# Performance work log

Measured on AMD Instinct MI355X. Metric: run time of the kernel, lower is better.

## Reference

```python
import jax, jax.numpy as jnp
import numpy as np

# Module hyperparameters (from init_kwargs)
B, C, E, T = 8, 128, 128, 128          # batch, in_channels, embedding(freq), time
O, G, KW, KS = 256, 4, 9, 1            # out_channels, groups, kernel_width, kernel_stride
D = C // G                              # kernel depth per group = 32
N = O // G                              # filters per group = 64
AH, AS = 2, 2                           # activate_height, activate_stride
NEG_SLOPE = 0.01                        # nn.LeakyReLU default


def setup_inputs() -> dict:
    key = jax.random.key(0)
    kx, kw = jax.random.split(key)
    x = jax.random.normal(kx, (B, C, E, T), dtype=jnp.float32)
    # xavier_uniform over (O, D, E, KW): fan_in = D*E*KW, fan_out = O*E*KW
    fan_in, fan_out = D * E * KW, O * E * KW
    limit = float(np.sqrt(6.0 / (fan_in + fan_out)))
    weight = jax.random.uniform(kw, (O, D, E, KW), dtype=jnp.float32,
                                minval=-limit, maxval=limit)
    return {"x": x, "weight": weight}


def reference(x, weight):
    b, c, e, t = x.shape
    # --- symmetric-ish zero pad along time so unfold yields exactly t windows ---
    pad = (t - 1) * KS - t + KW
    xp = jnp.pad(x, ((0, 0), (0, 0), (0, 0), (pad // 2, (pad + 1) // 2)))
    # --- unfold: windows of size KW at stride KS -> (b, c, e, t, KW) ---
    idx = jnp.arange(t)[:, None] * KS + jnp.arange(KW)[None, :]  # (t, KW)
    xu = xp[..., idx]                                            # (b, c, e, t, KW)
    # --- grouped linear-conv: instead of materializing (b,t,g,n,d,e,KW), contract d,KW ---
    xu = xu.reshape(b, G, D, e, t, KW)                 # (b, g, d, e, t, w)
    wr = weight.reshape(G, N, D, e, KW)                # (g, n, d, e, w)
    # z[b,g,n,e,t] = sum_{d,w} xu * wr  (the all-ones conv sums over d and full width w)
    z = jnp.einsum('bgdetw,gndew->bgnet', xu, wr).reshape(b, O, e, t)
    # --- all-ones conv height pooling: kernel AH, stride AS over e (valid) ---
    f_out = (e - AH) // AS + 1
    cs = jnp.cumsum(z, axis=2)
    cs = jnp.concatenate([jnp.zeros_like(cs[:, :, :1]), cs], axis=2)  # prefix sums
    pos = jnp.arange(f_out) * AS
    pooled = cs[:, :, pos + AH, :] - cs[:, :, pos, :]   # (b, O, f_out, t)
    # --- LeakyReLU ---
    y = jnp.where(pooled >= 0, pooled, NEG_SLOPE * pooled)
    return y  # (b, o, f_out, t), matching 'b o f t'
```

## Files before the change

kernel.cpp:

```cpp
#include <hip/hip_runtime.h>
#include <cstddef>

typedef __attribute__((ext_vector_type(8))) short short8v;
typedef __attribute__((ext_vector_type(4))) float f32x4;

__device__ __forceinline__ unsigned short f2bf(float f) {
    unsigned u = __float_as_uint(f);
    u = (u + 0x7FFFu + ((u >> 16) & 1u)) >> 16;
    return (unsigned short)u;
}

__global__ __launch_bounds__(256) void prep_w(const float* __restrict__ w,
                                              unsigned short* __restrict__ wb)
{
    const int o   = blockIdx.x;
    const int tid = threadIdx.x;
    __shared__ unsigned short ls[36864];
    const float* wo = w + (size_t)o * 36864;

    for (int i = 0; i < 36; ++i) {
        int idx4 = tid + i * 256;
        float4 v = reinterpret_cast<const float4*>(wo)[idx4];
        int f0 = idx4 * 4;
        int d  = f0 / 1152;
        int sw = (d & 31) << 1;
        int s0 = f0 ^ sw;
        ushort2 p0; p0.x = f2bf(v.x); p0.y = f2bf(v.y);
        ushort2 p1; p1.x = f2bf(v.z); p1.y = f2bf(v.w);
        *reinterpret_cast<ushort2*>(&ls[s0])     = p0;
        *reinterpret_cast<ushort2*>(&ls[s0 ^ 2]) = p1;
    }
    __syncthreads();

    const int g = o >> 6, n = o & 63;
    for (int i = 0; i < 18; ++i) {
        int c  = tid + i * 256;
        int q0 = c * 8;
        int e  = q0 / 288;
        int r  = q0 - e * 288;
        int wi = r >> 5;
        int d0 = r & 31;
        short8v vv;
        #pragma unroll
        for (int j = 0; j < 8; ++j) {
            int d = d0 + j;
            int fq = 1152 * d + 9 * e + wi;
            vv[j] = (short)ls[fq ^ ((d & 31) << 1)];
        }
        size_t oi = (((size_t)(g * 128 + e) * 64 + n) * 288 + (size_t)r);
        *reinterpret_cast<short8v*>(&wb[oi]) = vv;
    }
}

__global__ __launch_bounds__(256, 2) void lconv_mfma(const float* __restrict__ x,
                                                     const unsigned short* __restrict__ wb,
                                                     float* __restrict__ out)
{
    int bid = blockIdx.x;
    int c   = (bid & 7) * 256 + (bid >> 3);
    const int b = c & 7;
    const int f = (c >> 3) & 63;
    const int g = c >> 9;
    const int e0 = 2 * f;

    const int tid  = threadIdx.x;
    const int lane = tid & 63;
    const int wv   = tid >> 6;
    const int li   = lane & 15;
    const int hi   = lane >> 4;

    __shared__ __align__(16) unsigned short xs[2 * 144 * 40];
    __shared__ __align__(16) unsigned short ws[64 * 288];

    #pragma unroll
    for (int i = 0; i < 8; ++i) {
        int r   = tid + i * 256;
        int e   = r >> 10;
        int rem = r & 1023;
        int d   = rem >> 5;
        int t4  = rem & 31;
        const float4 v = *reinterpret_cast<const float4*>(
            &x[(((size_t)(b * 128 + g * 32 + d)) * 128 + (e0 + e)) * 128 + t4 * 4]);
        int tp0 = t4 * 4 + 4;
        unsigned short* p = &xs[(e * 144 + tp0) * 40 + d];
        p[0]   = f2bf(v.x);
        p[40]  = f2bf(v.y);
        p[80]  = f2bf(v.z);
        p[120] = f2bf(v.w);
    }
    {
        int p2 = tid;
        for (int i = 0; i < 2; ++i, p2 += 256) {
            int e = p2 >> 8;
            int j = (p2 >> 5) & 7;
            int d = p2 & 31;
            int tp = (j < 4) ? j : (128 + j);
            xs[(e * 144 + tp) * 40 + d] = 0;
        }
    }

    f32x4 acc[4][2];
    #pragma unroll
    for (int nt = 0; nt < 4; ++nt)
        #pragma unroll
        for (int tt = 0; tt < 2; ++tt)
            acc[nt][tt] = (f32x4){0.f, 0.f, 0.f, 0.f};

    for (int ec = 0; ec < 2; ++ec) {
        __syncthreads();
        const unsigned short* src = wb + (size_t)((g * 128) + e0 + ec) * (64 * 288);
        #pragma unroll
        for (int i = 0; i < 9; ++i) {
            int u = tid + i * 256;
            *reinterpret_cast<short8v*>(&ws[u * 8]) =
                *reinterpret_cast<const short8v*>(&src[u * 8]);
        }
        __syncthreads();

        #pragma unroll 3
        for (int w9 = 0; w9 < 9; ++w9) {
            short8v wa[4];
            #pragma unroll
            for (int nt = 0; nt < 4; ++nt)
                wa[nt] = *reinterpret_cast<const short8v*>(
                    &ws[(nt * 16 + li) * 288 + w9 * 32 + hi * 8]);

            short8v bx[2];
            #pragma unroll
            for (int tt = 0; tt < 2; ++tt) {
                int tp = wv * 32 + tt * 16 + li + w9;
                bx[tt] = *reinterpret_cast<const short8v*>(
                    &xs[(ec * 144 + tp) * 40 + hi * 8]);
            }

            #pragma unroll
            for (int nt = 0; nt < 4; ++nt)
                #pragma unroll
                for (int tt = 0; tt < 2; ++tt)
                    acc[nt][tt] = __builtin_amdgcn_mfma_f32_16x16x32_bf16(
                        wa[nt], bx[tt], acc[nt][tt], 0, 0, 0);
        }
    }

    #pragma unroll
    for (int nt = 0; nt < 4; ++nt) {
        #pragma unroll
        for (int tt = 0; tt < 2; ++tt) {
            #pragma unroll
            for (int j = 0; j < 4; ++j) {
                float v = acc[nt][tt][j];
                v = (v >= 0.f) ? v : 0.01f * v;
                int n = nt * 16 + hi * 4 + j;
                int t = wv * 32 + tt * 16 + li;
                out[(((size_t)(b * 256 + g * 64 + n)) * 64 + f) * 128 + t] = v;
            }
        }
    }
}

extern "C" void kernel_launch(void* const* d_in, const int* in_sizes, int n_in,
                              void* d_out, int out_size, void* d_ws, size_t ws_size,
                              hipStream_t stream)
{
    const float* x = (const float*)d_in[0];
    const float* w = (const float*)d_in[1];
    float* out = (float*)d_out;
    unsigned short* wb = (unsigned short*)d_ws;

    hipLaunchKernelGGL(prep_w, dim3(256), dim3(256), 0, stream, w, wb);
    hipLaunchKernelGGL(lconv_mfma, dim3(2048), dim3(256), 0, stream, x, wb, out);
}
```

Baseline: 61.70 us.

## Pre-layout weights into MFMA fragment order and stream them from global into registers

Result: slower. 77.69 us (+25.9%).

```diff
diff --git a/kernel.cpp b/kernel.cpp
--- a/kernel.cpp
+++ b/kernel.cpp
@@ -2,6 +2,7 @@
 #include <cstddef>
 
 typedef __attribute__((ext_vector_type(8))) short short8v;
+typedef __attribute__((ext_vector_type(4))) short short4v;
 typedef __attribute__((ext_vector_type(4))) float f32x4;
 
 __device__ __forceinline__ unsigned short f2bf(float f) {
@@ -13,46 +14,46 @@
 __global__ __launch_bounds__(256) void prep_w(const float* __restrict__ w,
                                               unsigned short* __restrict__ wb)
 {
-    const int o   = blockIdx.x;
+    const int g  = blockIdx.x >> 6;
+    const int f  = blockIdx.x & 63;
+    const int e0 = 2 * f;
     const int tid = threadIdx.x;
-    __shared__ unsigned short ls[36864];
-    const float* wo = w + (size_t)o * 36864;
+    __shared__ unsigned short ls[64 * 580];
 
-    for (int i = 0; i < 36; ++i) {
-        int idx4 = tid + i * 256;
-        float4 v = reinterpret_cast<const float4*>(wo)[idx4];
-        int f0 = idx4 * 4;
-        int d  = f0 / 1152;
-        int sw = (d & 31) << 1;
-        int s0 = f0 ^ sw;
-        ushort2 p0; p0.x = f2bf(v.x); p0.y = f2bf(v.y);
-        ushort2 p1; p1.x = f2bf(v.z); p1.y = f2bf(v.w);
-        *reinterpret_cast<ushort2*>(&ls[s0])     = p0;
-        *reinterpret_cast<ushort2*>(&ls[s0 ^ 2]) = p1;
+    #pragma unroll 4
+    for (int i = 0; i < 72; ++i) {
+        int fl  = tid + i * 256;
+        int od  = fl / 9;
+        int f2i = fl - od * 9;
+        int o_l = od >> 5;
+        int d   = od & 31;
+        const float2 v = *reinterpret_cast<const float2*>(
+            &w[(size_t)((g * 64 + o_l) * 32 + d) * 1152 + e0 * 9 + f2i * 2]);
+        ushort2 h; h.x = f2bf(v.x); h.y = f2bf(v.y);
+        *reinterpret_cast<ushort2*>(&ls[o_l * 580 + d * 18 + f2i * 2]) = h;
     }
     __syncthreads();
 
-    const int g = o >> 6, n = o & 63;
+    unsigned short* wo = wb + (size_t)(g * 64 + f) * 36864;
+    #pragma unroll 2
     for (int i = 0; i < 18; ++i) {
-        int c  = tid + i * 256;
-        int q0 = c * 8;
-        int e  = q0 / 288;
-        int r  = q0 - e * 288;
-        int wi = r >> 5;
-        int d0 = r & 31;
+        int oc   = tid + i * 256;
+        int ks   = oc >> 8;
+        int nt   = (oc >> 6) & 3;
+        int lane = oc & 63;
+        int li = lane & 15, hi = lane >> 4;
+        int ec = (ks >= 9) ? 1 : 0;
+        int w9 = ks - 9 * ec;
+        int o_l = nt * 16 + li;
         short8v vv;
         #pragma unroll
-        for (int j = 0; j < 8; ++j) {
-            int d = d0 + j;
-            int fq = 1152 * d + 9 * e + wi;
-            vv[j] = (short)ls[fq ^ ((d & 31) << 1)];
-        }
-        size_t oi = (((size_t)(g * 128 + e) * 64 + n) * 288 + (size_t)r);
-        *reinterpret_cast<short8v*>(&wb[oi]) = vv;
+        for (int j = 0; j < 8; ++j)
+            vv[j] = (short)ls[o_l * 580 + (hi * 8 + j) * 18 + ec * 9 + w9];
+        *reinterpret_cast<short8v*>(&wo[(size_t)oc * 8]) = vv;
     }
 }
 
-__global__ __launch_bounds__(256, 2) void lconv_mfma(const float* __restrict__ x,
+__global__ __launch_bounds__(128, 3) void lconv_mfma(const float* __restrict__ x,
                                                      const unsigned short* __restrict__ wb,
                                                      float* __restrict__ out)
 {
@@ -65,94 +66,93 @@
 
     const int tid  = threadIdx.x;
     const int lane = tid & 63;
-    const int wv   = tid >> 6;
+    const int th   = tid >> 6;
     const int li   = lane & 15;
     const int hi   = lane >> 4;
 
-    __shared__ __align__(16) unsigned short xs[2 * 144 * 40];
-    __shared__ __align__(16) unsigned short ws[64 * 288];
+    __shared__ __align__(16) unsigned short xs[2 * 136 * 40];
 
+    const int t = tid;
     #pragma unroll
-    for (int i = 0; i < 8; ++i) {
-        int r   = tid + i * 256;
-        int e   = r >> 10;
-        int rem = r & 1023;
-        int d   = rem >> 5;
-        int t4  = rem & 31;
-        const float4 v = *reinterpret_cast<const float4*>(
-            &x[(((size_t)(b * 128 + g * 32 + d)) * 128 + (e0 + e)) * 128 + t4 * 4]);
-        int tp0 = t4 * 4 + 4;
-        unsigned short* p = &xs[(e * 144 + tp0) * 40 + d];
-        p[0]   = f2bf(v.x);
-        p[40]  = f2bf(v.y);
-        p[80]  = f2bf(v.z);
-        p[120] = f2bf(v.w);
+    for (int i = 0; i < 16; ++i) {
+        int dhi = i & 7;
+        int e   = i >> 3;
+        const float* xp = &x[(size_t)((b * 128 + g * 32 + dhi * 4) * 128 + (e0 + e)) * 128 + t];
+        float v0 = xp[0];
+        float v1 = xp[128 * 128];
+        float v2 = xp[2 * 128 * 128];
+        float v3 = xp[3 * 128 * 128];
+        short4v hq;
+        hq[0] = (short)f2bf(v0); hq[1] = (short)f2bf(v1);
+        hq[2] = (short)f2bf(v2); hq[3] = (short)f2bf(v3);
+        *reinterpret_cast<short4v*>(&xs[(e * 136 + t + 4) * 40 + dhi * 4]) = hq;
     }
     {
-        int p2 = tid;
-        for (int i = 0; i < 2; ++i, p2 += 256) {
-            int e = p2 >> 8;
-            int j = (p2 >> 5) & 7;
-            int d = p2 & 31;
-            int tp = (j < 4) ? j : (128 + j);
-            xs[(e * 144 + tp) * 40 + d] = 0;
-        }
+        int e  = tid >> 6;
+        int r  = (tid >> 3) & 7;
+        int dq = tid & 7;
+        int tp = (r < 4) ? r : (128 + r);
+        short4v z = {0, 0, 0, 0};
+        *reinterpret_cast<short4v*>(&xs[(e * 136 + tp) * 40 + dq * 4]) = z;
     }
+    __syncthreads();
 
-    f32x4 acc[4][2];
+    const unsigned short* wsl = wb + (size_t)(g * 64 + f) * 36864;
+
+    f32x4 acc[4][4];
     #pragma unroll
     for (int nt = 0; nt < 4; ++nt)
         #pragma unroll
-        for (int tt = 0; tt < 2; ++tt)
+        for (int tt = 0; tt < 4; ++tt)
             acc[nt][tt] = (f32x4){0.f, 0.f, 0.f, 0.f};
 
-    for (int ec = 0; ec < 2; ++ec) {
-        __syncthreads();
-        const unsigned short* src = wb + (size_t)((g * 128) + e0 + ec) * (64 * 288);
+    short8v A[3][4];
+    #pragma unroll
+    for (int p = 0; p < 2; ++p)
         #pragma unroll
-        for (int i = 0; i < 9; ++i) {
-            int u = tid + i * 256;
-            *reinterpret_cast<short8v*>(&ws[u * 8]) =
-                *reinterpret_cast<const short8v*>(&src[u * 8]);
-        }
-        __syncthreads();
+        for (int nt = 0; nt < 4; ++nt)
+            A[p][nt] = *reinterpret_cast<const short8v*>(
+                &wsl[(size_t)(p * 4 + nt) * 512 + lane * 8]);
 
-        #pragma unroll 3
-        for (int w9 = 0; w9 < 9; ++w9) {
-            short8v wa[4];
+    #pragma unroll
+    for (int ks = 0; ks < 18; ++ks) {
+        const int cur = ks % 3;
+        if (ks < 16) {
+            const int ld = (ks + 2) % 3;
             #pragma unroll
             for (int nt = 0; nt < 4; ++nt)
-                wa[nt] = *reinterpret_cast<const short8v*>(
-                    &ws[(nt * 16 + li) * 288 + w9 * 32 + hi * 8]);
+                A[ld][nt] = *reinterpret_cast<const short8v*>(
+                    &wsl[(size_t)((ks + 2) * 4 + nt) * 512 + lane * 8]);
+        }
+        const int ec = (ks >= 9) ? 1 : 0;
+        const int w9 = ks - 9 * ec;
 
-            short8v bx[2];
+        short8v Bf[4];
+        #pragma unroll
+        for (int tt = 0; tt < 4; ++tt) {
+            int tp = th * 64 + tt * 16 + li + w9;
+            Bf[tt] = *reinterpret_cast<const short8v*>(
+                &xs[(ec * 136 + tp) * 40 + hi * 8]);
+        }
+        #pragma unroll
+        for (int nt = 0; nt < 4; ++nt)
             #pragma unroll
-            for (int tt = 0; tt < 2; ++tt) {
-                int tp = wv * 32 + tt * 16 + li + w9;
-                bx[tt] = *reinterpret_cast<const short8v*>(
-                    &xs[(ec * 144 + tp) * 40 + hi * 8]);
-            }
-
-            #pragma unroll
-            for (int nt = 0; nt < 4; ++nt)
-                #pragma unroll
-                for (int tt = 0; tt < 2; ++tt)
-                    acc[nt][tt] = __builtin_amdgcn_mfma_f32_16x16x32_bf16(
-                        wa[nt], bx[tt], acc[nt][tt], 0, 0, 0);
-        }
+            for (int tt = 0; tt < 4; ++tt)
+                acc[nt][tt] = __builtin_amdgcn_mfma_f32_16x16x32_bf16(
+                    A[cur][nt], Bf[tt], acc[nt][tt], 0, 0, 0);
     }
 
     #pragma unroll
     for (int nt = 0; nt < 4; ++nt) {
         #pragma unroll
-        for (int tt = 0; tt < 2; ++tt) {
+        for (int tt = 0; tt < 4; ++tt) {
             #pragma unroll
             for (int j = 0; j < 4; ++j) {
                 float v = acc[nt][tt][j];
                 v = (v >= 0.f) ? v : 0.01f * v;
-                int n = nt * 16 + hi * 4 + j;
-                int t = wv * 32 + tt * 16 + li;
-                out[(((size_t)(b * 256 + g * 64 + n)) * 64 + f) * 128 + t] = v;
+                int n  = nt * 16 + hi * 4 + j;
+                int tc = th * 64 + tt * 16 + li;
+                out[(((size_t)(b * 256 + g * 64 + n)) * 64 + f) * 128 + tc] = v;
             }
         }
     }
@@ -168,5 +168,5 @@
     unsigned short* wb = (unsigned short*)d_ws;
 
     hipLaunchKernelGGL(prep_w, dim3(256), dim3(256), 0, stream, w, wb);
-    hipLaunchKernelGGL(lconv_mfma, dim3(2048), dim3(256), 0, stream, x, wb, out);
+    hipLaunchKernelGGL(lconv_mfma, dim3(2048), dim3(128), 0, stream, x, wb, out);
 }
```

## Process two batches per block to reuse staged weight tiles

Applied to the files above, without the earlier changes.

Result: faster. 51.65 us (-16.3%).

```diff
diff --git a/kernel.cpp b/kernel.cpp
--- a/kernel.cpp
+++ b/kernel.cpp
@@ -2,6 +2,7 @@
 #include <cstddef>
 
 typedef __attribute__((ext_vector_type(8))) short short8v;
+typedef __attribute__((ext_vector_type(4))) short short4v;
 typedef __attribute__((ext_vector_type(4))) float f32x4;
 
 __device__ __forceinline__ unsigned short f2bf(float f) {
@@ -57,102 +58,109 @@
                                                      float* __restrict__ out)
 {
     int bid = blockIdx.x;
-    int c   = (bid & 7) * 256 + (bid >> 3);
-    const int b = c & 7;
-    const int f = (c >> 3) & 63;
-    const int g = c >> 9;
+    int lid = (bid & 7) * 128 + (bid >> 3);
+    const int bp = lid & 3;
+    const int f  = (lid >> 2) & 63;
+    const int g  = lid >> 8;
     const int e0 = 2 * f;
 
     const int tid  = threadIdx.x;
     const int lane = tid & 63;
     const int wv   = tid >> 6;
+    const int bl   = wv & 1;
+    const int th   = wv >> 1;
     const int li   = lane & 15;
     const int hi   = lane >> 4;
 
-    __shared__ __align__(16) unsigned short xs[2 * 144 * 40];
-    __shared__ __align__(16) unsigned short ws[64 * 288];
+    __shared__ __align__(16) unsigned short xs[2 * 136 * 40];
+    __shared__ __align__(16) unsigned short As[64 * 288];
 
-    #pragma unroll
-    for (int i = 0; i < 8; ++i) {
-        int r   = tid + i * 256;
-        int e   = r >> 10;
-        int rem = r & 1023;
-        int d   = rem >> 5;
-        int t4  = rem & 31;
-        const float4 v = *reinterpret_cast<const float4*>(
-            &x[(((size_t)(b * 128 + g * 32 + d)) * 128 + (e0 + e)) * 128 + t4 * 4]);
-        int tp0 = t4 * 4 + 4;
-        unsigned short* p = &xs[(e * 144 + tp0) * 40 + d];
-        p[0]   = f2bf(v.x);
-        p[40]  = f2bf(v.y);
-        p[80]  = f2bf(v.z);
-        p[120] = f2bf(v.w);
-    }
-    {
-        int p2 = tid;
-        for (int i = 0; i < 2; ++i, p2 += 256) {
-            int e = p2 >> 8;
-            int j = (p2 >> 5) & 7;
-            int d = p2 & 31;
-            int tp = (j < 4) ? j : (128 + j);
-            xs[(e * 144 + tp) * 40 + d] = 0;
-        }
+    if (tid < 128) {
+        int blz = tid >> 6;
+        int r   = (tid >> 3) & 7;
+        int dq  = tid & 7;
+        int tp  = (r < 4) ? r : (128 + r);
+        short4v z = {0, 0, 0, 0};
+        *reinterpret_cast<short4v*>(&xs[(blz * 136 + tp) * 40 + dq * 4]) = z;
     }
 
-    f32x4 acc[4][2];
+    f32x4 acc[4][4];
     #pragma unroll
     for (int nt = 0; nt < 4; ++nt)
         #pragma unroll
-        for (int tt = 0; tt < 2; ++tt)
+        for (int tt = 0; tt < 4; ++tt)
             acc[nt][tt] = (f32x4){0.f, 0.f, 0.f, 0.f};
+
+    const int t  = tid & 127;
+    const int z  = tid >> 7;
 
     for (int ec = 0; ec < 2; ++ec) {
         __syncthreads();
-        const unsigned short* src = wb + (size_t)((g * 128) + e0 + ec) * (64 * 288);
+
         #pragma unroll
-        for (int i = 0; i < 9; ++i) {
-            int u = tid + i * 256;
-            *reinterpret_cast<short8v*>(&ws[u * 8]) =
-                *reinterpret_cast<const short8v*>(&src[u * 8]);
+        for (int i = 0; i < 8; ++i) {
+            int u   = z * 8 + i;
+            int bl2 = u >> 3;
+            int dq  = u & 7;
+            const float* xp = &x[(size_t)(((bp * 2 + bl2) * 128 + g * 32 + dq * 4) * 128
+                                          + (e0 + ec)) * 128 + t];
+            float v0 = xp[0];
+            float v1 = xp[128 * 128];
+            float v2 = xp[2 * 128 * 128];
+            float v3 = xp[3 * 128 * 128];
+            short4v hq;
+            hq[0] = (short)f2bf(v0); hq[1] = (short)f2bf(v1);
+            hq[2] = (short)f2bf(v2); hq[3] = (short)f2bf(v3);
+            *reinterpret_cast<short4v*>(&xs[(bl2 * 136 + t + 4) * 40 + dq * 4]) = hq;
+        }
+        {
+            const unsigned short* src = wb + (size_t)((g * 128) + e0 + ec) * (64 * 288);
+            #pragma unroll
+            for (int i = 0; i < 9; ++i) {
+                int u = tid + i * 256;
+                *reinterpret_cast<short8v*>(&As[u * 8]) =
+                    *reinterpret_cast<const short8v*>(&src[u * 8]);
+            }
         }
         __syncthreads();
 
-        #pragma unroll 3
+        #pragma unroll
         for (int w9 = 0; w9 < 9; ++w9) {
-            short8v wa[4];
+            short8v Af[4];
             #pragma unroll
             for (int nt = 0; nt < 4; ++nt)
-                wa[nt] = *reinterpret_cast<const short8v*>(
-                    &ws[(nt * 16 + li) * 288 + w9 * 32 + hi * 8]);
+                Af[nt] = *reinterpret_cast<const short8v*>(
+                    &As[(nt * 16 + li) * 288 + w9 * 32 + hi * 8]);
 
-            short8v bx[2];
+            short8v Bf[4];
             #pragma unroll
-            for (int tt = 0; tt < 2; ++tt) {
-                int tp = wv * 32 + tt * 16 + li + w9;
-                bx[tt] = *reinterpret_cast<const short8v*>(
-                    &xs[(ec * 144 + tp) * 40 + hi * 8]);
+            for (int tt = 0; tt < 4; ++tt) {
+                int tp = th * 64 + tt * 16 + li + w9;
+                Bf[tt] = *reinterpret_cast<const short8v*>(
+                    &xs[(bl * 136 + tp) * 40 + hi * 8]);
             }
 
             #pragma unroll
             for (int nt = 0; nt < 4; ++nt)
                 #pragma unroll
-                for (int tt = 0; tt < 2; ++tt)
+                for (int tt = 0; tt < 4; ++tt)
                     acc[nt][tt] = __builtin_amdgcn_mfma_f32_16x16x32_bf16(
-                        wa[nt], bx[tt], acc[nt][tt], 0, 0, 0);
+                        Af[nt], Bf[tt], acc[nt][tt], 0, 0, 0);
         }
     }
 
+    const int b = bp * 2 + bl;
     #pragma unroll
     for (int nt = 0; nt < 4; ++nt) {
         #pragma unroll
-        for (int tt = 0; tt < 2; ++tt) {
+        for (int tt = 0; tt < 4; ++tt) {
             #pragma unroll
             for (int j = 0; j < 4; ++j) {
                 float v = acc[nt][tt][j];
                 v = (v >= 0.f) ? v : 0.01f * v;
-                int n = nt * 16 + hi * 4 + j;
-                int t = wv * 32 + tt * 16 + li;
-                out[(((size_t)(b * 256 + g * 64 + n)) * 64 + f) * 128 + t] = v;
+                int n  = nt * 16 + hi * 4 + j;
+                int tc = th * 64 + tt * 16 + li;
+                out[(((size_t)(b * 256 + g * 64 + n)) * 64 + f) * 128 + tc] = v;
             }
         }
     }
@@ -168,5 +176,5 @@
     unsigned short* wb = (unsigned short*)d_ws;
 
     hipLaunchKernelGGL(prep_w, dim3(256), dim3(256), 0, stream, w, wb);
-    hipLaunchKernelGGL(lconv_mfma, dim3(2048), dim3(256), 0, stream, x, wb, out);
+    hipLaunchKernelGGL(lconv_mfma, dim3(1024), dim3(256), 0, stream, x, wb, out);
 }
```
